# Kernel optimization log

Hardware: AMD Instinct MI355X
Metric: run time of the kernel (lower is better)

## Reference

```python
import jax, jax.numpy as jnp
import numpy as np

N_PTS = 262144      # 512x512 coordinate grid
N_HEADS = 16
HID = 256
N_HID_LAYERS = 3
IN_F = 2
OUT_F = 3
PE_L = 10                  # NeRF positional-encoding frequencies
PE_DIM = 2 * IN_F * PE_L   # sin+cos per freq per coord = 40
CAP = N_PTS // N_HEADS     # balanced partition: points per head


def positional_encoding(x):
    # x: [..., IN_F] -> [..., PE_DIM]
    freqs = (2.0 ** jnp.arange(PE_L, dtype=x.dtype)) * jnp.pi          # [L]
    ang = x[..., None, :] * freqs[:, None]                              # [..., L, IN_F]
    pe = jnp.concatenate([jnp.sin(ang), jnp.cos(ang)], axis=-1)        # [..., L, 2*IN_F]
    return pe.reshape(*x.shape[:-1], PE_DIM)


def setup_inputs() -> dict:
    key = jax.random.key(0)
    ks = jax.random.split(key, 5)
    # Balanced random segment map (equivalent to the module's segment_weight),
    # converted to the static routing table the torch loop recomputes each step:
    # head_idx[h] = where(segment_weight == h)
    rng = np.random.default_rng(0)
    seg = rng.permutation(np.arange(N_PTS) % N_HEADS)
    head_idx = np.stack([np.where(seg == h)[0] for h in range(N_HEADS)]).astype(np.int32)  # [H, CAP]

    coords = jax.random.uniform(ks[0], (1, N_PTS, IN_F), minval=-1.0, maxval=1.0)

    def he(k, shape, fan_in):
        return jax.random.normal(k, shape, dtype=jnp.float32) * np.float32(np.sqrt(2.0 / fan_in))

    W_in = he(ks[1], (N_HEADS, PE_DIM, HID), PE_DIM)
    b_in = jnp.zeros((N_HEADS, HID), jnp.float32)
    W_hid = he(ks[2], (N_HEADS, N_HID_LAYERS, HID, HID), HID)
    b_hid = jnp.zeros((N_HEADS, N_HID_LAYERS, HID), jnp.float32)
    W_out = he(ks[3], (N_HEADS, HID, OUT_F), HID)
    b_out = jnp.zeros((N_HEADS, OUT_F), jnp.float32)

    return dict(coords=coords, head_idx=jnp.asarray(head_idx),
                W_in=W_in, b_in=b_in, W_hid=W_hid, b_hid=b_hid,
                W_out=W_out, b_out=b_out)


def reference(coords, head_idx, W_in, b_in, W_hid, b_hid, W_out, b_out):
    # --- dispatch: gather each head's points (torch: coords[:, index, :]) ---
    coords_h = coords[0][head_idx]                                      # [H, CAP, IN_F]
    # --- per-head MLP (relu_MLP with positional embedding) ---
    h = jax.nn.relu(jnp.einsum('hcd,hdf->hcf', positional_encoding(coords_h), W_in)
                    + b_in[:, None, :])                                 # [H, CAP, HID]
    for l in range(N_HID_LAYERS):
        h = jax.nn.relu(jnp.einsum('hcf,hfg->hcg', h, W_hid[:, l])
                        + b_hid[:, l, None, :])
    out_h = jnp.einsum('hcf,hfo->hco', h, W_out) + b_out[:, None, :]    # [H, CAP, OUT_F]
    # --- combine: scatter per-head outputs back (torch: output_final[0, index, :] = out) ---
    out_final = jnp.zeros((1, N_PTS, OUT_F), coords.dtype)
    out_final = out_final.at[0, head_idx.reshape(-1)].set(out_h.reshape(-1, OUT_F))
    return (out_final, coords)
```

## Files before the change

kernel.cpp:

```cpp
#include <hip/hip_runtime.h>

typedef unsigned short u16;
typedef unsigned int   u32;
typedef __bf16  bf16x8 __attribute__((ext_vector_type(8)));
typedef float   f32x16 __attribute__((ext_vector_type(16)));

#define CAP      16384
#define L0_ELS   (256*48)
#define HID_ELS  65536
#define OUT_ELS  8192
#define HEAD_WS  (L0_ELS + 3*HID_ELS + OUT_ELS)
#define HID_OFF  L0_ELS
#define OUT_OFF  (L0_ELS + 3*HID_ELS)

union F8 { u32 u[4]; bf16x8 v; };

__device__ __forceinline__ u16 f2b(float f) {
  u32 u = __float_as_uint(f); u += 0x7fffu + ((u >> 16) & 1u); return (u16)(u >> 16);
}
__device__ __forceinline__ u32 packbf2(float a, float b) {
  u32 ua = __float_as_uint(a); ua += 0x7fffu + ((ua >> 16) & 1u);
  u32 ub = __float_as_uint(b); ub += 0x7fffu + ((ub >> 16) & 1u);
  return (ua >> 16) | (ub & 0xffff0000u);
}
__device__ __forceinline__ f32x16 mfma16(bf16x8 a, bf16x8 b, f32x16 c) {
  return __builtin_amdgcn_mfma_f32_32x32x16_bf16(a, b, c, 0, 0, 0);
}

__device__ __forceinline__ void stage_now(const u16* g, short* l, int bytes, int tid) {
  for (int base = tid * 16; base < bytes; base += 8192)
    *(uint4*)((char*)l + base) = *(const uint4*)((const char*)g + base);
}
__device__ __forceinline__ void stage_ld(const u16* g, int bytes, int tid, uint4 st[4]) {
#pragma unroll
  for (int r = 0; r < 4; ++r) {
    const int base = tid * 16 + r * 8192;
    if (base < bytes) st[r] = *(const uint4*)((const char*)g + base);
  }
}
__device__ __forceinline__ void stage_st(short* l, int bytes, int tid, const uint4 st[4]) {
#pragma unroll
  for (int r = 0; r < 4; ++r) {
    const int base = tid * 16 + r * 8192;
    if (base < bytes) *(uint4*)((char*)l + base) = st[r];
  }
}

__device__ __forceinline__ bf16x8 frag64(const short* sl, int i, int t, int n, int hh) {
  return *(const bf16x8*)((const char*)sl + ((((2*t + hh) << 6) + 32*i + n) << 4));
}
__device__ __forceinline__ bf16x8 fragO(const short* sl, int t, int n, int hh) {
  return *(const bf16x8*)((const char*)sl + ((((2*t + hh) << 5) + n) << 4));
}

__device__ __forceinline__ void epi_core(const float cb[16], int hh, F8& t0, F8& t1) {
  u32 P[8];
#pragma unroll
  for (int i = 0; i < 8; ++i)
    P[i] = packbf2(fmaxf(cb[2*i], 0.f), fmaxf(cb[2*i+1], 0.f));
  u32 s0 = hh ? P[0] : P[2], s1 = hh ? P[1] : P[3];
  u32 s2 = hh ? P[4] : P[6], s3 = hh ? P[5] : P[7];
  u32 x0 = __shfl_xor(s0, 32, 64), x1 = __shfl_xor(s1, 32, 64);
  u32 x2 = __shfl_xor(s2, 32, 64), x3 = __shfl_xor(s3, 32, 64);
  t0.u[0] = hh ? x0 : P[0]; t0.u[1] = hh ? x1 : P[1];
  t0.u[2] = hh ? P[2] : x0; t0.u[3] = hh ? P[3] : x1;
  t1.u[0] = hh ? x2 : P[4]; t1.u[1] = hh ? x3 : P[5];
  t1.u[2] = hh ? P[6] : x2; t1.u[3] = hh ? P[7] : x3;
}
__device__ __forceinline__ void epilogue(f32x16 c, int hh, F8& t0, F8& t1) {
  float cb[16];
#pragma unroll
  for (int e = 0; e < 16; ++e) cb[e] = c[e];
  epi_core(cb, hh, t0, t1);
}
__device__ __forceinline__ void epilogueB(f32x16 c, const float4 bb[4], int hh, F8& t0, F8& t1) {
  float cb[16];
#pragma unroll
  for (int e = 0; e < 16; ++e) cb[e] = c[e] + ((const float*)bb)[e];
  epi_core(cb, hh, t0, t1);
}

__global__ void prep_hid(const float* __restrict__ W_hid, u16* __restrict__ ws) {
  __shared__ u16 tile[64 * 72];
  const int b = blockIdx.x;
  const int kband = b & 3, q = (b >> 2) & 3, l = (b >> 4) % 3, head = b / 48;
  const int t = threadIdx.x;
  const int kl = t >> 2, rg = t & 3;
  const float* src = W_hid + (((head*3 + l)*256 + kband*64 + kl) << 8) + q*64 + rg*16;
  u16* dt = &tile[kl*72 + rg*16];
#pragma unroll
  for (int m = 0; m < 4; ++m) {
    float4 v = *(const float4*)(src + m*4);
    ushort4 o; o.x = f2b(v.x); o.y = f2b(v.y); o.z = f2b(v.z); o.w = f2b(v.w);
    *(ushort4*)(dt + m*4) = o;
  }
  __syncthreads();
  u16* dbase = ws + head*HEAD_WS + HID_OFF + l*HID_ELS + q*16384 + (kband << 12);
#pragma unroll
  for (int p = 0; p < 2; ++p) {
    const int idx = t + p*256;
    const int cl = idx >> 6, rq = idx & 63;
    u16 v8[8];
#pragma unroll
    for (int j = 0; j < 8; ++j) v8[j] = tile[(cl*8 + j)*72 + rq];
    uint4 o;
    o.x = (u32)v8[0] | ((u32)v8[1] << 16); o.y = (u32)v8[2] | ((u32)v8[3] << 16);
    o.z = (u32)v8[4] | ((u32)v8[5] << 16); o.w = (u32)v8[6] | ((u32)v8[7] << 16);
    *(uint4*)(dbase + ((cl << 6) + rq) * 8) = o;
  }
}

__global__ void prep_small(const float* __restrict__ W_in, const float* __restrict__ b_in,
                           const float* __restrict__ W_out, u16* __restrict__ ws,
                           const uint4* __restrict__ csrc, uint4* __restrict__ cdst) {
  if (blockIdx.x >= 160) {
    const int i = (blockIdx.x - 160) * 256 + threadIdx.x;
    cdst[i] = csrc[i];
    return;
  }
  const int r = blockIdx.x * 256 + threadIdx.x;
  const int head = r / 2560, f = r % 2560;
  u16 v[8]; int dst;
  if (f < 1536) {
    const int q = f / 384, g = f % 384;
    const int c = g >> 6, row = g & 63, nn = q*64 + row, k0 = c*8;
#pragma unroll
    for (int j = 0; j < 8; ++j) {
      const int k = k0 + j;
      v[j] = (k < 40) ? f2b(W_in[head*10240 + (k << 8) + nn])
           : (k == 40) ? f2b(b_in[(head << 8) + nn]) : (u16)0;
    }
    dst = head*HEAD_WS + q*3072 + g*8;
  } else {
    const int f2 = f - 1536;
    const int c = f2 >> 5, nn = f2 & 31, k0 = c*8;
#pragma unroll
    for (int j = 0; j < 8; ++j)
      v[j] = (nn < 3) ? f2b(W_out[head*768 + (k0 + j)*3 + nn]) : (u16)0;
    dst = head*HEAD_WS + OUT_OFF + f2*8;
  }
  uint4 o;
  o.x = (u32)v[0] | ((u32)v[1] << 16); o.y = (u32)v[2] | ((u32)v[3] << 16);
  o.z = (u32)v[4] | ((u32)v[5] << 16); o.w = (u32)v[6] | ((u32)v[7] << 16);
  *(uint4*)(ws + dst) = o;
}

__launch_bounds__(512, 2)
__global__ void mlp_main(const float* __restrict__ coords, const int* __restrict__ head_idx,
                         const float* __restrict__ b_hid, const float* __restrict__ b_out,
                         const u16* __restrict__ ws, float* __restrict__ out) {
  __shared__ short ring[2 * 16384];
  const int tid = threadIdx.x;
  const int lane = tid & 63, wv = tid >> 6;
  const int n = lane & 31, hh = lane >> 5;
  const int head = blockIdx.x & 15, chunk = blockIdx.x >> 4;
  const u16* wsh = ws + head * HEAD_WS;

  stage_now(wsh + 0*3072, ring,          6144, tid);
  stage_now(wsh + 1*3072, ring + 16384,  6144, tid);

  const int pt = chunk*256 + wv*32 + n;
  const int g  = head_idx[head*CAP + pt];
  const float2 cxy = *(const float2*)(coords + 2*g);
  const float xs = cxy.x, ys = cxy.y;
  const float bo0 = b_out[head*3+0], bo1 = b_out[head*3+1], bo2 = b_out[head*3+2];

  F8 pe[3];
#pragma unroll
  for (int t = 0; t < 3; ++t) {
    float e[8];
#pragma unroll
    for (int half = 0; half < 2; ++half) {
      const int l = 4*t + 2*hh + half;
      if (l < 10) {
        const float fr = 3.14159265358979323846f * (float)(1 << l);
        float s1, c1, s2, c2;
        sincosf(xs * fr, &s1, &c1);
        sincosf(ys * fr, &s2, &c2);
        e[4*half+0] = s1; e[4*half+1] = s2; e[4*half+2] = c1; e[4*half+3] = c2;
      } else {
        e[4*half+0] = (l == 10) ? 1.0f : 0.0f;
        e[4*half+1] = 0.f; e[4*half+2] = 0.f; e[4*half+3] = 0.f;
      }
    }
    pe[t].u[0] = packbf2(e[0], e[1]); pe[t].u[1] = packbf2(e[2], e[3]);
    pe[t].u[2] = packbf2(e[4], e[5]); pe[t].u[3] = packbf2(e[6], e[7]);
  }

  F8 act0[16], act1[16];
  __syncthreads();

#pragma unroll
  for (int rp = 0; rp < 4; ++rp) {
    short* sl = ring + (rp & 1) * 16384;
    f32x16 acc0 = (f32x16)0.f, acc1 = (f32x16)0.f;
#pragma unroll
    for (int t = 0; t < 3; ++t) {
      acc0 = mfma16(frag64(sl, 0, t, n, hh), pe[t].v, acc0);
      acc1 = mfma16(frag64(sl, 1, t, n, hh), pe[t].v, acc1);
    }
    __syncthreads();
    const u16* src = (rp < 2) ? (wsh + (rp + 2)*3072) : (wsh + HID_OFF + (rp - 2)*16384);
    const int bytes = (rp < 2) ? 6144 : 32768;
    uint4 st[4];
    stage_ld(src, bytes, tid, st);
    epilogue(acc0, hh, act0[4*rp+0], act0[4*rp+1]);
    epilogue(acc1, hh, act0[4*rp+2], act0[4*rp+3]);
    stage_st(sl, bytes, tid, st);
  }

  auto hid_layer = [&](const float* bias, F8 (&ain)[16], F8 (&aout)[16],
                       const u16* j0, const u16* j1, const u16* j2, const u16* j3,
                       int b2, int b3) {
    const u16* jsrc[4] = { j0, j1, j2, j3 };
    const int  jb[4]   = { 32768, 32768, b2, b3 };
#pragma unroll
    for (int rp = 0; rp < 4; ++rp) {
      short* sl = ring + (rp & 1) * 16384;
      f32x16 acc0 = (f32x16)0.f, acc1 = (f32x16)0.f;
#pragma unroll
      for (int t = 0; t < 16; ++t) {
        acc0 = mfma16(frag64(sl, 0, t, n, hh), ain[t].v, acc0);
        acc1 = mfma16(frag64(sl, 1, t, n, hh), ain[t].v, acc1);
      }
      __syncthreads();
      uint4 st[4];
      if (jb[rp] > 0) stage_ld(jsrc[rp], jb[rp], tid, st);
      float4 bb0[4], bb1[4];
#pragma unroll
      for (int g2 = 0; g2 < 4; ++g2) {
        bb0[g2] = *(const float4*)(bias + 64*rp +      8*g2 + 4*hh);
        bb1[g2] = *(const float4*)(bias + 64*rp + 32 + 8*g2 + 4*hh);
      }
      epilogueB(acc0, bb0, hh, aout[4*rp+0], aout[4*rp+1]);
      epilogueB(acc1, bb1, hh, aout[4*rp+2], aout[4*rp+3]);
      if (jb[rp] > 0) stage_st(sl, jb[rp], tid, st);
    }
  };

  const u16* hb = wsh + HID_OFF;
  hid_layer(b_hid + (head*3+0)*256, act0, act1,
            hb + 2*16384, hb + 3*16384, hb + HID_ELS, hb + HID_ELS + 16384, 32768, 32768);
  hid_layer(b_hid + (head*3+1)*256, act1, act0,
            hb + HID_ELS + 2*16384, hb + HID_ELS + 3*16384,
            hb + 2*HID_ELS, hb + 2*HID_ELS + 16384, 32768, 32768);
  hid_layer(b_hid + (head*3+2)*256, act0, act1,
            hb + 2*HID_ELS + 2*16384, hb + 2*HID_ELS + 3*16384,
            wsh + OUT_OFF, (const u16*)0, 16384, 0);

  f32x16 acc = (f32x16)0.f;
#pragma unroll
  for (int t = 0; t < 16; ++t)
    acc = mfma16(fragO(ring, t, n, hh), act1[t].v, acc);
  if (hh == 0) {
    const long base = (long)g * 3;
    out[base + 0] = acc[0] + bo0;
    out[base + 1] = acc[1] + bo1;
    out[base + 2] = acc[2] + bo2;
  }
}

extern "C" void kernel_launch(void* const* d_in, const int* in_sizes, int n_in,
                              void* d_out, int out_size, void* d_ws, size_t ws_size,
                              hipStream_t stream) {
  const float* coords   = (const float*)d_in[0];
  const int*   head_idx = (const int*)d_in[1];
  const float* W_in     = (const float*)d_in[2];
  const float* b_in     = (const float*)d_in[3];
  const float* W_hid    = (const float*)d_in[4];
  const float* b_hid    = (const float*)d_in[5];
  const float* W_out    = (const float*)d_in[6];
  const float* b_out    = (const float*)d_in[7];
  float* out = (float*)d_out;
  u16*   ws  = (u16*)d_ws;
  if (ws_size < (size_t)HEAD_WS * 16 * sizeof(u16)) return;

  prep_hid  <<<dim3(768), dim3(256), 0, stream>>>(W_hid, ws);
  prep_small<<<dim3(672), dim3(256), 0, stream>>>(W_in, b_in, W_out, ws,
                                                  (const uint4*)coords, (uint4*)(out + 786432));
  mlp_main  <<<dim3(1024), dim3(512), 0, stream>>>(coords, head_idx, b_hid, b_out, ws, out);
}
```

Baseline: 233.0 us.

## Halve weight staging slots to 32-column panels and merge prep kernels

The weight ring in LDS shrinks from two 64-column slots to two 32-column slots (32KB total). Each layer now runs 8 stages of one MFMA accumulator instead of 4 stages of two, and the prep kernel lays weights out in matching 32-row panels. The two prep kernels are merged into a single launch, and launch bounds request more resident blocks. The aim is higher occupancy and one less launch, at the cost of twice as many barriers per layer and less MFMA work between them.

```diff
diff --git a/kernel.cpp b/kernel.cpp
--- a/kernel.cpp
+++ b/kernel.cpp
@@ -6,12 +6,13 @@
 typedef float   f32x16 __attribute__((ext_vector_type(16)));
 
 #define CAP      16384
-#define L0_ELS   (256*48)
+#define L0_ELS   12288
 #define HID_ELS  65536
 #define OUT_ELS  8192
 #define HEAD_WS  (L0_ELS + 3*HID_ELS + OUT_ELS)
 #define HID_OFF  L0_ELS
 #define OUT_OFF  (L0_ELS + 3*HID_ELS)
+#define SLOT     8192
 
 union F8 { u32 u[4]; bf16x8 v; };
 
@@ -31,25 +32,22 @@
   for (int base = tid * 16; base < bytes; base += 8192)
     *(uint4*)((char*)l + base) = *(const uint4*)((const char*)g + base);
 }
-__device__ __forceinline__ void stage_ld(const u16* g, int bytes, int tid, uint4 st[4]) {
-#pragma unroll
-  for (int r = 0; r < 4; ++r) {
+__device__ __forceinline__ void stage_ld2(const u16* g, int bytes, int tid, uint4 st[2]) {
+#pragma unroll
+  for (int r = 0; r < 2; ++r) {
     const int base = tid * 16 + r * 8192;
     if (base < bytes) st[r] = *(const uint4*)((const char*)g + base);
   }
 }
-__device__ __forceinline__ void stage_st(short* l, int bytes, int tid, const uint4 st[4]) {
-#pragma unroll
-  for (int r = 0; r < 4; ++r) {
+__device__ __forceinline__ void stage_st2(short* l, int bytes, int tid, const uint4 st[2]) {
+#pragma unroll
+  for (int r = 0; r < 2; ++r) {
     const int base = tid * 16 + r * 8192;
     if (base < bytes) *(uint4*)((char*)l + base) = st[r];
   }
 }
 
-__device__ __forceinline__ bf16x8 frag64(const short* sl, int i, int t, int n, int hh) {
-  return *(const bf16x8*)((const char*)sl + ((((2*t + hh) << 6) + 32*i + n) << 4));
-}
-__device__ __forceinline__ bf16x8 fragO(const short* sl, int t, int n, int hh) {
+__device__ __forceinline__ bf16x8 frag32(const short* sl, int t, int n, int hh) {
   return *(const bf16x8*)((const char*)sl + ((((2*t + hh) << 5) + n) << 4));
 }
 
@@ -80,57 +78,59 @@
   epi_core(cb, hh, t0, t1);
 }
 
-__global__ void prep_hid(const float* __restrict__ W_hid, u16* __restrict__ ws) {
+__global__ void prep(const float* __restrict__ W_in, const float* __restrict__ b_in,
+                     const float* __restrict__ W_hid, const float* __restrict__ W_out,
+                     u16* __restrict__ ws,
+                     const uint4* __restrict__ csrc, uint4* __restrict__ cdst) {
   __shared__ u16 tile[64 * 72];
-  const int b = blockIdx.x;
-  const int kband = b & 3, q = (b >> 2) & 3, l = (b >> 4) % 3, head = b / 48;
   const int t = threadIdx.x;
-  const int kl = t >> 2, rg = t & 3;
-  const float* src = W_hid + (((head*3 + l)*256 + kband*64 + kl) << 8) + q*64 + rg*16;
-  u16* dt = &tile[kl*72 + rg*16];
-#pragma unroll
-  for (int m = 0; m < 4; ++m) {
-    float4 v = *(const float4*)(src + m*4);
-    ushort4 o; o.x = f2b(v.x); o.y = f2b(v.y); o.z = f2b(v.z); o.w = f2b(v.w);
-    *(ushort4*)(dt + m*4) = o;
-  }
-  __syncthreads();
-  u16* dbase = ws + head*HEAD_WS + HID_OFF + l*HID_ELS + q*16384 + (kband << 12);
-#pragma unroll
-  for (int p = 0; p < 2; ++p) {
-    const int idx = t + p*256;
-    const int cl = idx >> 6, rq = idx & 63;
-    u16 v8[8];
-#pragma unroll
-    for (int j = 0; j < 8; ++j) v8[j] = tile[(cl*8 + j)*72 + rq];
-    uint4 o;
-    o.x = (u32)v8[0] | ((u32)v8[1] << 16); o.y = (u32)v8[2] | ((u32)v8[3] << 16);
-    o.z = (u32)v8[4] | ((u32)v8[5] << 16); o.w = (u32)v8[6] | ((u32)v8[7] << 16);
-    *(uint4*)(dbase + ((cl << 6) + rq) * 8) = o;
-  }
-}
-
-__global__ void prep_small(const float* __restrict__ W_in, const float* __restrict__ b_in,
-                           const float* __restrict__ W_out, u16* __restrict__ ws,
-                           const uint4* __restrict__ csrc, uint4* __restrict__ cdst) {
-  if (blockIdx.x >= 160) {
-    const int i = (blockIdx.x - 160) * 256 + threadIdx.x;
+  if (blockIdx.x < 768) {
+    const int b = blockIdx.x;
+    const int kband = b & 3, q = (b >> 2) & 3, l = (b >> 4) % 3, head = b / 48;
+    const int kl = t >> 2, rg = t & 3;
+    const float* src = W_hid + (((head*3 + l)*256 + kband*64 + kl) << 8) + q*64 + rg*16;
+    u16* dt = &tile[kl*72 + rg*16];
+#pragma unroll
+    for (int m = 0; m < 4; ++m) {
+      float4 v = *(const float4*)(src + m*4);
+      ushort4 o; o.x = f2b(v.x); o.y = f2b(v.y); o.z = f2b(v.z); o.w = f2b(v.w);
+      *(ushort4*)(dt + m*4) = o;
+    }
+    __syncthreads();
+    u16* lbase = ws + head*HEAD_WS + HID_OFF + l*HID_ELS;
+#pragma unroll
+    for (int p = 0; p < 2; ++p) {
+      const int idx = t + p*256;
+      const int cl = idx >> 6, rq = idx & 63;
+      const int e = (q << 1) | (rq >> 5), r32 = rq & 31, kc = kband*8 + cl;
+      u16 v8[8];
+#pragma unroll
+      for (int j = 0; j < 8; ++j) v8[j] = tile[(cl*8 + j)*72 + rq];
+      uint4 o;
+      o.x = (u32)v8[0] | ((u32)v8[1] << 16); o.y = (u32)v8[2] | ((u32)v8[3] << 16);
+      o.z = (u32)v8[4] | ((u32)v8[5] << 16); o.w = (u32)v8[6] | ((u32)v8[7] << 16);
+      *(uint4*)(lbase + e*SLOT + ((kc << 5) + r32) * 8) = o;
+    }
+    return;
+  }
+  if (blockIdx.x >= 928) {
+    const int i = (blockIdx.x - 928) * 256 + t;
     cdst[i] = csrc[i];
     return;
   }
-  const int r = blockIdx.x * 256 + threadIdx.x;
+  const int r = (blockIdx.x - 768) * 256 + t;
   const int head = r / 2560, f = r % 2560;
   u16 v[8]; int dst;
   if (f < 1536) {
-    const int q = f / 384, g = f % 384;
-    const int c = g >> 6, row = g & 63, nn = q*64 + row, k0 = c*8;
+    const int e = f / 192, g = f % 192;
+    const int c = g >> 5, row = g & 31, nn = e*32 + row, k0 = c*8;
 #pragma unroll
     for (int j = 0; j < 8; ++j) {
       const int k = k0 + j;
       v[j] = (k < 40) ? f2b(W_in[head*10240 + (k << 8) + nn])
            : (k == 40) ? f2b(b_in[(head << 8) + nn]) : (u16)0;
     }
-    dst = head*HEAD_WS + q*3072 + g*8;
+    dst = head*HEAD_WS + e*1536 + g*8;
   } else {
     const int f2 = f - 1536;
     const int c = f2 >> 5, nn = f2 & 31, k0 = c*8;
@@ -145,19 +145,20 @@
   *(uint4*)(ws + dst) = o;
 }
 
-__launch_bounds__(512, 2)
+__launch_bounds__(512, 8)
 __global__ void mlp_main(const float* __restrict__ coords, const int* __restrict__ head_idx,
                          const float* __restrict__ b_hid, const float* __restrict__ b_out,
                          const u16* __restrict__ ws, float* __restrict__ out) {
-  __shared__ short ring[2 * 16384];
+  __shared__ short ring[2 * SLOT];
   const int tid = threadIdx.x;
   const int lane = tid & 63, wv = tid >> 6;
   const int n = lane & 31, hh = lane >> 5;
   const int head = blockIdx.x & 15, chunk = blockIdx.x >> 4;
   const u16* wsh = ws + head * HEAD_WS;
-
-  stage_now(wsh + 0*3072, ring,          6144, tid);
-  stage_now(wsh + 1*3072, ring + 16384,  6144, tid);
+  const u16* hb  = wsh + HID_OFF;
+
+  stage_now(wsh + 0*1536, ring,        3072, tid);
+  stage_now(wsh + 1*1536, ring + SLOT, 3072, tid);
 
   const int pt = chunk*256 + wv*32 + n;
   const int g  = head_idx[head*CAP + pt];
@@ -191,67 +192,55 @@
   __syncthreads();
 
 #pragma unroll
-  for (int rp = 0; rp < 4; ++rp) {
-    short* sl = ring + (rp & 1) * 16384;
-    f32x16 acc0 = (f32x16)0.f, acc1 = (f32x16)0.f;
-#pragma unroll
-    for (int t = 0; t < 3; ++t) {
-      acc0 = mfma16(frag64(sl, 0, t, n, hh), pe[t].v, acc0);
-      acc1 = mfma16(frag64(sl, 1, t, n, hh), pe[t].v, acc1);
-    }
+  for (int e = 0; e < 8; ++e) {
+    short* sl = ring + (e & 1) * SLOT;
+    f32x16 acc = (f32x16)0.f;
+#pragma unroll
+    for (int t = 0; t < 3; ++t)
+      acc = mfma16(frag32(sl, t, n, hh), pe[t].v, acc);
     __syncthreads();
-    const u16* src = (rp < 2) ? (wsh + (rp + 2)*3072) : (wsh + HID_OFF + (rp - 2)*16384);
-    const int bytes = (rp < 2) ? 6144 : 32768;
-    uint4 st[4];
-    stage_ld(src, bytes, tid, st);
-    epilogue(acc0, hh, act0[4*rp+0], act0[4*rp+1]);
-    epilogue(acc1, hh, act0[4*rp+2], act0[4*rp+3]);
-    stage_st(sl, bytes, tid, st);
+    const u16* src = (e < 6) ? (wsh + (e + 2)*1536) : (hb + (e - 6)*SLOT);
+    const int bytes = (e < 6) ? 3072 : 16384;
+    uint4 st[2];
+    stage_ld2(src, bytes, tid, st);
+    epilogue(acc, hh, act0[2*e], act0[2*e+1]);
+    stage_st2(sl, bytes, tid, st);
   }
 
   auto hid_layer = [&](const float* bias, F8 (&ain)[16], F8 (&aout)[16],
-                       const u16* j0, const u16* j1, const u16* j2, const u16* j3,
-                       int b2, int b3) {
-    const u16* jsrc[4] = { j0, j1, j2, j3 };
-    const int  jb[4]   = { 32768, 32768, b2, b3 };
-#pragma unroll
-    for (int rp = 0; rp < 4; ++rp) {
-      short* sl = ring + (rp & 1) * 16384;
-      f32x16 acc0 = (f32x16)0.f, acc1 = (f32x16)0.f;
-#pragma unroll
-      for (int t = 0; t < 16; ++t) {
-        acc0 = mfma16(frag64(sl, 0, t, n, hh), ain[t].v, acc0);
-        acc1 = mfma16(frag64(sl, 1, t, n, hh), ain[t].v, acc1);
-      }
+                       const u16* lay, const u16* n0, const u16* n1, int nb7) {
+#pragma unroll
+    for (int e = 0; e < 8; ++e) {
+      short* sl = ring + (e & 1) * SLOT;
+      f32x16 acc = (f32x16)0.f;
+#pragma unroll
+      for (int t = 0; t < 16; ++t)
+        acc = mfma16(frag32(sl, t, n, hh), ain[t].v, acc);
       __syncthreads();
-      uint4 st[4];
-      if (jb[rp] > 0) stage_ld(jsrc[rp], jb[rp], tid, st);
-      float4 bb0[4], bb1[4];
-#pragma unroll
-      for (int g2 = 0; g2 < 4; ++g2) {
-        bb0[g2] = *(const float4*)(bias + 64*rp +      8*g2 + 4*hh);
-        bb1[g2] = *(const float4*)(bias + 64*rp + 32 + 8*g2 + 4*hh);
-      }
-      epilogueB(acc0, bb0, hh, aout[4*rp+0], aout[4*rp+1]);
-      epilogueB(acc1, bb1, hh, aout[4*rp+2], aout[4*rp+3]);
-      if (jb[rp] > 0) stage_st(sl, jb[rp], tid, st);
+      const u16* src = (e < 6) ? (lay + (e + 2)*SLOT) : (e == 6 ? n0 : n1);
+      const int bytes = (e < 7) ? 16384 : nb7;
+      uint4 st[2];
+      if (bytes) stage_ld2(src, bytes, tid, st);
+      float4 bb[4];
+#pragma unroll
+      for (int g2 = 0; g2 < 4; ++g2)
+        bb[g2] = *(const float4*)(bias + 32*e + 8*g2 + 4*hh);
+      epilogueB(acc, bb, hh, aout[2*e], aout[2*e+1]);
+      if (bytes) stage_st2(sl, bytes, tid, st);
     }
   };
 
-  const u16* hb = wsh + HID_OFF;
-  hid_layer(b_hid + (head*3+0)*256, act0, act1,
-            hb + 2*16384, hb + 3*16384, hb + HID_ELS, hb + HID_ELS + 16384, 32768, 32768);
-  hid_layer(b_hid + (head*3+1)*256, act1, act0,
-            hb + HID_ELS + 2*16384, hb + HID_ELS + 3*16384,
-            hb + 2*HID_ELS, hb + 2*HID_ELS + 16384, 32768, 32768);
-  hid_layer(b_hid + (head*3+2)*256, act0, act1,
-            hb + 2*HID_ELS + 2*16384, hb + 2*HID_ELS + 3*16384,
-            wsh + OUT_OFF, (const u16*)0, 16384, 0);
+  hid_layer(b_hid + (head*3+0)*256, act0, act1, hb,
+            hb + HID_ELS, hb + HID_ELS + SLOT, 16384);
+  hid_layer(b_hid + (head*3+1)*256, act1, act0, hb + HID_ELS,
+            hb + 2*HID_ELS, hb + 2*HID_ELS + SLOT, 16384);
+  hid_layer(b_hid + (head*3+2)*256, act0, act1, hb + 2*HID_ELS,
+            wsh + OUT_OFF, (const u16*)0, 0);
 
   f32x16 acc = (f32x16)0.f;
 #pragma unroll
   for (int t = 0; t < 16; ++t)
-    acc = mfma16(fragO(ring, t, n, hh), act1[t].v, acc);
+    acc = mfma16(frag32(ring, t, n, hh), act1[t].v, acc);
   if (hh == 0) {
     const long base = (long)g * 3;
     out[base + 0] = acc[0] + bo0;
@@ -275,8 +264,7 @@
   u16*   ws  = (u16*)d_ws;
   if (ws_size < (size_t)HEAD_WS * 16 * sizeof(u16)) return;
 
-  prep_hid  <<<dim3(768), dim3(256), 0, stream>>>(W_hid, ws);
-  prep_small<<<dim3(672), dim3(256), 0, stream>>>(W_in, b_in, W_out, ws,
-                                                  (const uint4*)coords, (uint4*)(out + 786432));
-  mlp_main  <<<dim3(1024), dim3(512), 0, stream>>>(coords, head_idx, b_hid, b_out, ws, out);
-}
+  prep<<<dim3(1440), dim3(256), 0, stream>>>(W_in, b_in, W_hid, W_out, ws,
+                                             (const uint4*)coords, (uint4*)(out + 786432));
+  mlp_main<<<dim3(1024), dim3(512), 0, stream>>>(coords, head_idx, b_hid, b_out, ws, out);
+}
```

Measured after the change: 856.9 us. +267.7%, slower.
